# Optimization experiments

Measured on AMD Instinct MI355X. Metric: run time of the kernel, lower is better.

## Reference

```python
import jax, jax.numpy as jnp
import numpy as np

BLOCK = 64  # NF4 block size
SCALING = 32.0 / 16.0  # lora_alpha / r

# Standard NF4 (normal-float 4-bit) codebook, 16 levels
NF4_TABLE = jnp.asarray([
    -1.0, -0.6961928009986877, -0.5250730514526367, -0.39491748809814453,
    -0.28444138169288635, -0.18477343022823334, -0.09105003625154495, 0.0,
    0.07958029955625534, 0.16093020141124725, 0.24611230194568634,
    0.33791524171829224, 0.44070982933044434, 0.5626170039176941,
    0.7229568362236023, 1.0], dtype=jnp.float32)


def dequant_nf4(codes, scales):
    # codes: [out, in] int in [0,16); scales: [out, in//BLOCK] float
    out_f, in_f = codes.shape
    w = NF4_TABLE[codes].reshape(out_f, in_f // BLOCK, BLOCK)
    w = w * scales[:, :, None]
    return w.reshape(out_f, in_f)


def setup_inputs() -> dict:
    key = jax.random.key(0)
    k1, k2, k3, k4, k5 = jax.random.split(key, 5)
    B, S, D_in, D_out, R = 4, 2048, 4096, 4096, 16
    x = jax.random.normal(k1, (B, S, D_in), dtype=jnp.float32)
    codes = jax.random.randint(k2, (D_out, D_in), 0, 16, dtype=jnp.int32)
    scales = jax.random.uniform(k3, (D_out, D_in // BLOCK), dtype=jnp.float32)
    lora_A = jax.random.normal(k4, (R, D_in), dtype=jnp.float32) * (1.0 / np.sqrt(D_in))
    lora_B = jax.random.normal(k5, (D_out, R), dtype=jnp.float32) * 0.02
    return {"x": x, "codes": codes, "scales": scales,
            "lora_A": lora_A, "lora_B": lora_B}


def reference(x, codes, scales, lora_A, lora_B):
    # Base path: F.linear(x, dequant(W))  -> x @ W^T
    W = dequant_nf4(codes, scales)            # [out, in]
    base = jnp.einsum('bsd,od->bso', x, W)    # [B, S, out]
    # LoRA path (dropout p=0.0 -> identity): (x @ A^T) @ B^T * scaling
    lora = jnp.einsum('bsr,or->bso', jnp.einsum('bsd,rd->bsr', x, lora_A), lora_B)
    return base + lora * SCALING
```

## Files before the change

### kernel.cpp

```cpp
#include <hip/hip_runtime.h>
#include <hip/hip_bf16.h>

typedef __attribute__((ext_vector_type(8))) short short8;
typedef __attribute__((ext_vector_type(4))) short short4v;
typedef __attribute__((ext_vector_type(4))) float floatx4;

#define M_DIM 8192
#define N_DIM 4096
#define K_DIM 4096
#define BK 64

__device__ __constant__ float NF4_TAB[16] = {
    -1.0f, -0.6961928009986877f, -0.5250730514526367f, -0.39491748809814453f,
    -0.28444138169288635f, -0.18477343022823334f, -0.09105003625154495f, 0.0f,
    0.07958029955625534f, 0.16093020141124725f, 0.24611230194568634f,
    0.33791524171829224f, 0.44070982933044434f, 0.5626170039176941f,
    0.7229568362236023f, 1.0f};

__global__ __launch_bounds__(256)
void dequant_lora_kernel(const int* __restrict__ codes,
                         const float* __restrict__ scales,
                         const float* __restrict__ la,
                         const float* __restrict__ lb,
                         short4v* __restrict__ W) {
    __shared__ float tab[16];
    if (threadIdx.x < 16) tab[threadIdx.x] = NF4_TAB[threadIdx.x];
    __syncthreads();

    const int kb = blockIdx.x & 3;
    const int n0 = (blockIdx.x >> 2) << 4;
    const int k0 = kb * 1024 + threadIdx.x * 4;

    float4 a[16];
#pragma unroll
    for (int r = 0; r < 16; r++)
        a[r] = *(const float4*)(la + (size_t)r * K_DIM + k0);

#pragma unroll 4
    for (int i = 0; i < 16; i++) {
        const int n = n0 + i;
        int4 c = *(const int4*)(codes + (size_t)n * K_DIM + k0);
        float s = scales[(n << 6) + (k0 >> 6)];
        const float* bp = lb + (n << 4);
        float acc0 = 0.f, acc1 = 0.f, acc2 = 0.f, acc3 = 0.f;
#pragma unroll
        for (int r = 0; r < 16; r++) {
            float br = bp[r];
            acc0 += br * a[r].x;
            acc1 += br * a[r].y;
            acc2 += br * a[r].z;
            acc3 += br * a[r].w;
        }
        union { short4v v; __hip_bfloat16 h[4]; } u;
        u.h[0] = __float2bfloat16(tab[c.x] * s + 2.0f * acc0);
        u.h[1] = __float2bfloat16(tab[c.y] * s + 2.0f * acc1);
        u.h[2] = __float2bfloat16(tab[c.z] * s + 2.0f * acc2);
        u.h[3] = __float2bfloat16(tab[c.w] * s + 2.0f * acc3);
        W[((size_t)n * K_DIM + k0) >> 2] = u.v;
    }
}

__global__ void cast_x_kernel(const float* __restrict__ x,
                              short8* __restrict__ xb) {
    int g = blockIdx.x * blockDim.x + threadIdx.x;
    const float4* xp = (const float4*)(x + (size_t)g * 8);
    float4 v0 = xp[0], v1 = xp[1];
    union { short8 v; __hip_bfloat16 h[8]; } u;
    u.h[0] = __float2bfloat16(v0.x);
    u.h[1] = __float2bfloat16(v0.y);
    u.h[2] = __float2bfloat16(v0.z);
    u.h[3] = __float2bfloat16(v0.w);
    u.h[4] = __float2bfloat16(v1.x);
    u.h[5] = __float2bfloat16(v1.y);
    u.h[6] = __float2bfloat16(v1.z);
    u.h[7] = __float2bfloat16(v1.w);
    xb[g] = u.v;
}

#define GL2LDS(gsrc, ldst)                                                   \
    __builtin_amdgcn_global_load_lds(                                        \
        (const __attribute__((address_space(1))) void*)(gsrc),               \
        (__attribute__((address_space(3))) void*)(ldst), 16, 0, 0)


#define STAGE_A(D, H, T) do {                                                 \
    GL2LDS(gA0 + (size_t)((H) * 128) * K_DIM + (T) * BK,                      \
           ldsA + (D) * 32768 + (H) * 16384 + ldsw);                          \
    GL2LDS(gA0 + (size_t)((H) * 128 + 64) * K_DIM + (T) * BK,                 \
           ldsA + (D) * 32768 + (H) * 16384 + 8192 + ldsw);                   \
} while (0)

#define STAGE_B(D, H, T) do {                                                 \
    GL2LDS(gB0 + (size_t)((H) * 128) * K_DIM + (T) * BK,                      \
           ldsB + (D) * 32768 + (H) * 16384 + ldsw);                          \
    GL2LDS(gB0 + (size_t)((H) * 128 + 64) * K_DIM + (T) * BK,                 \
           ldsB + (D) * 32768 + (H) * 16384 + 8192 + ldsw);                   \
} while (0)

#define MFMA_Q(AF, BF, MB, NB) do {                                           \
    _Pragma("unroll") for (int mi_ = 0; mi_ < 4; mi_++)                       \
    _Pragma("unroll") for (int ni_ = 0; ni_ < 2; ni_++)                       \
    _Pragma("unroll") for (int ks_ = 0; ks_ < 2; ks_++)                       \
        acc[(MB) + mi_][(NB) + ni_] =                                         \
            __builtin_amdgcn_mfma_f32_16x16x32_bf16(                          \
                AF[mi_][ks_], BF[ni_][ks_], acc[(MB) + mi_][(NB) + ni_],      \
                0, 0, 0);                                                     \
} while (0)

#define LGKM0 asm volatile("s_waitcnt lgkmcnt(0)" ::: "memory")
#define VM4   asm volatile("s_waitcnt vmcnt(4)" ::: "memory")
#define VM0   asm volatile("s_waitcnt vmcnt(0)" ::: "memory")
#define VMNONE do {} while (0)

#define TILE(T, D, DOB, DOA, VM) do {                                         \
    short8 af0[4][2], af1[4][2], bf0[2][2], bf1[2][2];                        \
                                 \
    _Pragma("unroll") for (int mi_ = 0; mi_ < 4; mi_++) {                     \
        int o_ = (D) * 32768 + aoff + mi_ * 2048;                             \
        af0[mi_][0] = *(const short8*)(ldsA + o_);                            \
        af0[mi_][1] = *(const short8*)(ldsA + (o_ ^ 64));                     \
    }                                                                         \
    _Pragma("unroll") for (int ni_ = 0; ni_ < 2; ni_++) {                     \
        int o_ = (D) * 32768 + boff + ni_ * 2048;                             \
        bf0[ni_][0] = *(const short8*)(ldsB + o_);                            \
        bf0[ni_][1] = *(const short8*)(ldsB + (o_ ^ 64));                     \
    }                                                                         \
    if (DOB) STAGE_B((D) ^ 1, 0, (T) + 1);                                    \
    __builtin_amdgcn_s_barrier();                                             \
    LGKM0;                                                                    \
    __builtin_amdgcn_s_setprio(1);                                            \
    MFMA_Q(af0, bf0, 0, 0);                                                   \
    __builtin_amdgcn_s_setprio(0);                                            \
    __builtin_amdgcn_s_barrier();                                             \
                                          \
    _Pragma("unroll") for (int mi_ = 0; mi_ < 4; mi_++) {                     \
        int o_ = (D) * 32768 + aoff + 8192 + mi_ * 2048;                      \
        af1[mi_][0] = *(const short8*)(ldsA + o_);                            \
        af1[mi_][1] = *(const short8*)(ldsA + (o_ ^ 64));                     \
    }                                                                         \
    if (DOB) STAGE_B((D) ^ 1, 1, (T) + 1);                                    \
    __builtin_amdgcn_s_barrier();                                             \
    LGKM0;                                                                    \
    __builtin_amdgcn_s_setprio(1);                                            \
    MFMA_Q(af1, bf0, 4, 0);                                                   \
    __builtin_amdgcn_s_setprio(0);                                            \
    __builtin_amdgcn_s_barrier();                                             \
                                          \
    _Pragma("unroll") for (int ni_ = 0; ni_ < 2; ni_++) {                     \
        int o_ = (D) * 32768 + boff + 4096 + ni_ * 2048;                      \
        bf1[ni_][0] = *(const short8*)(ldsB + o_);                            \
        bf1[ni_][1] = *(const short8*)(ldsB + (o_ ^ 64));                     \
    }                                                                         \
    if (DOA) STAGE_A((D), 0, (T) + 2);                                        \
    __builtin_amdgcn_s_barrier();                                             \
    LGKM0;                                                                    \
    __builtin_amdgcn_s_setprio(1);                                            \
    MFMA_Q(af0, bf1, 0, 2);                                                   \
    __builtin_amdgcn_s_setprio(0);                                            \
    __builtin_amdgcn_s_barrier();                                             \
                       \
    if (DOA) STAGE_A((D), 1, (T) + 2);                                        \
    VM;                                                                       \
    __builtin_amdgcn_s_barrier();                                             \
    __builtin_amdgcn_s_setprio(1);                                            \
    MFMA_Q(af1, bf1, 4, 2);                                                   \
    __builtin_amdgcn_s_setprio(0);                                            \
    __builtin_amdgcn_s_barrier();                                             \
} while (0)

__global__ __launch_bounds__(512, 2)
void gemm_bt_kernel(const __hip_bfloat16* __restrict__ A,
                    const __hip_bfloat16* __restrict__ B,
                    float* __restrict__ C) {
    __shared__ __align__(16) char lds[131072];
    char* ldsA = (char*)lds;
    char* ldsB = (char*)lds + 65536;

    const int tid = threadIdx.x;
    const int wave = tid >> 6;
    const int lane = tid & 63;
    const int q = lane >> 4;
    const int t16 = lane & 15;
    const int wm = wave >> 2;
    const int wn = wave & 3;

    const int bid = blockIdx.x;
    const int swz = ((bid & 7) << 6) | (bid >> 3);
    const int bm0 = (swz >> 4) << 8;
    const int bn0 = (swz & 15) << 8;

    const int sw = (q ^ (t16 & 7)) << 4;
    const int aoff = (wm * 128 + t16) * 128 + sw;
    const int boff = (wn * 64 + t16) * 128 + sw;

    const int r0 = tid >> 3;
    const int c0 = ((tid & 7) ^ (r0 & 7)) << 3;
    const __hip_bfloat16* gA0 = A + (size_t)(bm0 + r0) * K_DIM + c0;
    const __hip_bfloat16* gB0 = B + (size_t)(bn0 + r0) * K_DIM + c0;
    const int ldsw = wave << 10;

    floatx4 acc[8][4] = {};

    STAGE_A(0, 0, 0); STAGE_A(0, 1, 0);
    STAGE_B(0, 0, 0); STAGE_B(0, 1, 0);
    STAGE_A(1, 0, 1); STAGE_A(1, 1, 1);
    VM4;
    __builtin_amdgcn_s_barrier();

#pragma unroll 1
    for (int tp = 0; tp < 31; ++tp) {
        const int t2 = tp << 1;
        TILE(t2, 0, 1, 1, VM4);
        TILE(t2 + 1, 1, 1, 1, VM4);
    }
    TILE(62, 0, 1, 0, VM0);
    TILE(63, 1, 0, 0, VMNONE);

#pragma unroll
    for (int mi = 0; mi < 8; mi++) {
        int row0 = bm0 + wm * 128 + mi * 16 + q * 4;
#pragma unroll
        for (int ni = 0; ni < 4; ni++) {
            int col = bn0 + wn * 64 + ni * 16 + t16;
            float* cp = C + (size_t)row0 * N_DIM + col;
#pragma unroll
            for (int r = 0; r < 4; r++) cp[(size_t)r * N_DIM] = acc[mi][ni][r];
        }
    }
}

extern "C" void kernel_launch(void* const* d_in, const int* in_sizes, int n_in,
                              void* d_out, int out_size, void* d_ws,
                              size_t ws_size, hipStream_t stream) {
    const float* x = (const float*)d_in[0];
    const int* codes = (const int*)d_in[1];
    const float* scales = (const float*)d_in[2];
    const float* loraA = (const float*)d_in[3];
    const float* loraB = (const float*)d_in[4];
    float* out = (float*)d_out;

    char* ws = (char*)d_ws;
    __hip_bfloat16* xb = (__hip_bfloat16*)ws;
    __hip_bfloat16* Wb = (__hip_bfloat16*)(ws + 67108864);

    dequant_lora_kernel<<<dim3(4 * (N_DIM / 16)), dim3(256), 0, stream>>>(
        codes, scales, loraA, loraB, (short4v*)Wb);
    cast_x_kernel<<<dim3((M_DIM * (K_DIM / 8)) / 256), dim3(256), 0, stream>>>(
        x, (short8*)xb);
    gemm_bt_kernel<<<dim3(512), dim3(512), 0, stream>>>(xb, Wb, out);
}
```

Before: 483.6 us.

## Prefetch next-tile LDS fragments in GEMM and merge prep kernels into one launch

The GEMM main loop now reads the next tile's first A and B fragments from LDS during the last MFMA quarter of the current tile. Each quarter's fragment read is moved one phase earlier, and the explicit lgkmcnt(0) waits are removed, so LDS latency can overlap MFMA work. The fragment registers are hoisted out of the tile macro so they persist across tiles, which raises register pressure. Separately, the dequant+LoRA kernel and the x-to-bf16 cast are merged into a single launch that branches on block index, saving one kernel launch and letting the two parts run concurrently.

After: 565.1 us. 16.9% more time.

```diff
diff --git a/kernel.cpp b/kernel.cpp
--- a/kernel.cpp
+++ b/kernel.cpp
@@ -18,63 +18,63 @@
     0.7229568362236023f, 1.0f};
 
 __global__ __launch_bounds__(256)
-void dequant_lora_kernel(const int* __restrict__ codes,
-                         const float* __restrict__ scales,
-                         const float* __restrict__ la,
-                         const float* __restrict__ lb,
-                         short4v* __restrict__ W) {
+void prep_kernel(const float* __restrict__ x, short8* __restrict__ xb,
+                 const int* __restrict__ codes,
+                 const float* __restrict__ scales,
+                 const float* __restrict__ la, const float* __restrict__ lb,
+                 short4v* __restrict__ W) {
     __shared__ float tab[16];
-    if (threadIdx.x < 16) tab[threadIdx.x] = NF4_TAB[threadIdx.x];
-    __syncthreads();
-
-    const int kb = blockIdx.x & 3;
-    const int n0 = (blockIdx.x >> 2) << 4;
-    const int k0 = kb * 1024 + threadIdx.x * 4;
-
-    float4 a[16];
-#pragma unroll
-    for (int r = 0; r < 16; r++)
-        a[r] = *(const float4*)(la + (size_t)r * K_DIM + k0);
+    const int bid = blockIdx.x;
+    if (bid < 1024) {
+        if (threadIdx.x < 16) tab[threadIdx.x] = NF4_TAB[threadIdx.x];
+        __syncthreads();
+
+        const int kb = bid & 3;
+        const int n0 = (bid >> 2) << 4;
+        const int k0 = kb * 1024 + threadIdx.x * 4;
+
+        float4 a[16];
+#pragma unroll
+        for (int r = 0; r < 16; r++)
+            a[r] = *(const float4*)(la + (size_t)r * K_DIM + k0);
 
 #pragma unroll 4
-    for (int i = 0; i < 16; i++) {
-        const int n = n0 + i;
-        int4 c = *(const int4*)(codes + (size_t)n * K_DIM + k0);
-        float s = scales[(n << 6) + (k0 >> 6)];
-        const float* bp = lb + (n << 4);
-        float acc0 = 0.f, acc1 = 0.f, acc2 = 0.f, acc3 = 0.f;
-#pragma unroll
-        for (int r = 0; r < 16; r++) {
-            float br = bp[r];
-            acc0 += br * a[r].x;
-            acc1 += br * a[r].y;
-            acc2 += br * a[r].z;
-            acc3 += br * a[r].w;
+        for (int i = 0; i < 16; i++) {
+            const int n = n0 + i;
+            int4 c = *(const int4*)(codes + (size_t)n * K_DIM + k0);
+            float s = scales[(n << 6) + (k0 >> 6)];
+            const float* bp = lb + (n << 4);
+            float acc0 = 0.f, acc1 = 0.f, acc2 = 0.f, acc3 = 0.f;
+#pragma unroll
+            for (int r = 0; r < 16; r++) {
+                float br = bp[r];
+                acc0 += br * a[r].x;
+                acc1 += br * a[r].y;
+                acc2 += br * a[r].z;
+                acc3 += br * a[r].w;
+            }
+            union { short4v v; __hip_bfloat16 h[4]; } u;
+            u.h[0] = __float2bfloat16(tab[c.x] * s + 2.0f * acc0);
+            u.h[1] = __float2bfloat16(tab[c.y] * s + 2.0f * acc1);
+            u.h[2] = __float2bfloat16(tab[c.z] * s + 2.0f * acc2);
+            u.h[3] = __float2bfloat16(tab[c.w] * s + 2.0f * acc3);
+            W[((size_t)n * K_DIM + k0) >> 2] = u.v;
         }
-        union { short4v v; __hip_bfloat16 h[4]; } u;
-        u.h[0] = __float2bfloat16(tab[c.x] * s + 2.0f * acc0);
-        u.h[1] = __float2bfloat16(tab[c.y] * s + 2.0f * acc1);
-        u.h[2] = __float2bfloat16(tab[c.z] * s + 2.0f * acc2);
-        u.h[3] = __float2bfloat16(tab[c.w] * s + 2.0f * acc3);
-        W[((size_t)n * K_DIM + k0) >> 2] = u.v;
+    } else {
+        const int g = (bid - 1024) * 256 + threadIdx.x;
+        const float4* xp = (const float4*)(x + (size_t)g * 8);
+        float4 v0 = xp[0], v1 = xp[1];
+        union { short8 v; __hip_bfloat16 h[8]; } u;
+        u.h[0] = __float2bfloat16(v0.x);
+        u.h[1] = __float2bfloat16(v0.y);
+        u.h[2] = __float2bfloat16(v0.z);
+        u.h[3] = __float2bfloat16(v0.w);
+        u.h[4] = __float2bfloat16(v1.x);
+        u.h[5] = __float2bfloat16(v1.y);
+        u.h[6] = __float2bfloat16(v1.z);
+        u.h[7] = __float2bfloat16(v1.w);
+        xb[g] = u.v;
     }
-}
-
-__global__ void cast_x_kernel(const float* __restrict__ x,
-                              short8* __restrict__ xb) {
-    int g = blockIdx.x * blockDim.x + threadIdx.x;
-    const float4* xp = (const float4*)(x + (size_t)g * 8);
-    float4 v0 = xp[0], v1 = xp[1];
-    union { short8 v; __hip_bfloat16 h[8]; } u;
-    u.h[0] = __float2bfloat16(v0.x);
-    u.h[1] = __float2bfloat16(v0.y);
-    u.h[2] = __float2bfloat16(v0.z);
-    u.h[3] = __float2bfloat16(v0.w);
-    u.h[4] = __float2bfloat16(v1.x);
-    u.h[5] = __float2bfloat16(v1.y);
-    u.h[6] = __float2bfloat16(v1.z);
-    u.h[7] = __float2bfloat16(v1.w);
-    xb[g] = u.v;
 }
 
 #define GL2LDS(gsrc, ldst)                                                   \
@@ -95,6 +95,38 @@
            ldsB + (D) * 32768 + (H) * 16384 + ldsw);                          \
     GL2LDS(gB0 + (size_t)((H) * 128 + 64) * K_DIM + (T) * BK,                 \
            ldsB + (D) * 32768 + (H) * 16384 + 8192 + ldsw);                   \
+} while (0)
+
+#define READ_AF0(D) do {                                                      \
+    _Pragma("unroll") for (int mi_ = 0; mi_ < 4; mi_++) {                     \
+        int o_ = (D) * 32768 + aoff + mi_ * 2048;                             \
+        af0[mi_][0] = *(const short8*)(ldsA + o_);                            \
+        af0[mi_][1] = *(const short8*)(ldsA + (o_ ^ 64));                     \
+    }                                                                         \
+} while (0)
+
+#define READ_AF1(D) do {                                                      \
+    _Pragma("unroll") for (int mi_ = 0; mi_ < 4; mi_++) {                     \
+        int o_ = (D) * 32768 + aoff + 8192 + mi_ * 2048;                      \
+        af1[mi_][0] = *(const short8*)(ldsA + o_);                            \
+        af1[mi_][1] = *(const short8*)(ldsA + (o_ ^ 64));                     \
+    }                                                                         \
+} while (0)
+
+#define READ_BF0(D) do {                                                      \
+    _Pragma("unroll") for (int ni_ = 0; ni_ < 2; ni_++) {                     \
+        int o_ = (D) * 32768 + boff + ni_ * 2048;                             \
+        bf0[ni_][0] = *(const short8*)(ldsB + o_);                            \
+        bf0[ni_][1] = *(const short8*)(ldsB + (o_ ^ 64));                     \
+    }                                                                         \
+} while (0)
+
+#define READ_BF1(D) do {                                                      \
+    _Pragma("unroll") for (int ni_ = 0; ni_ < 2; ni_++) {                     \
+        int o_ = (D) * 32768 + boff + 4096 + ni_ * 2048;                      \
+        bf1[ni_][0] = *(const short8*)(ldsB + o_);                            \
+        bf1[ni_][1] = *(const short8*)(ldsB + (o_ ^ 64));                     \
+    }                                                                         \
 } while (0)
 
 #define MFMA_Q(AF, BF, MB, NB) do {                                           \
@@ -107,61 +139,35 @@
                 0, 0, 0);                                                     \
 } while (0)
 
-#define LGKM0 asm volatile("s_waitcnt lgkmcnt(0)" ::: "memory")
 #define VM4   asm volatile("s_waitcnt vmcnt(4)" ::: "memory")
 #define VM0   asm volatile("s_waitcnt vmcnt(0)" ::: "memory")
 #define VMNONE do {} while (0)
 
-#define TILE(T, D, DOB, DOA, VM) do {                                         \
-    short8 af0[4][2], af1[4][2], bf0[2][2], bf1[2][2];                        \
-                                 \
-    _Pragma("unroll") for (int mi_ = 0; mi_ < 4; mi_++) {                     \
-        int o_ = (D) * 32768 + aoff + mi_ * 2048;                             \
-        af0[mi_][0] = *(const short8*)(ldsA + o_);                            \
-        af0[mi_][1] = *(const short8*)(ldsA + (o_ ^ 64));                     \
-    }                                                                         \
-    _Pragma("unroll") for (int ni_ = 0; ni_ < 2; ni_++) {                     \
-        int o_ = (D) * 32768 + boff + ni_ * 2048;                             \
-        bf0[ni_][0] = *(const short8*)(ldsB + o_);                            \
-        bf0[ni_][1] = *(const short8*)(ldsB + (o_ ^ 64));                     \
-    }                                                                         \
+#define TILE(T, D, DOB, DOA, VM, DOPF) do {                                   \
+    READ_AF1(D);                                                              \
     if (DOB) STAGE_B((D) ^ 1, 0, (T) + 1);                                    \
     __builtin_amdgcn_s_barrier();                                             \
-    LGKM0;                                                                    \
     __builtin_amdgcn_s_setprio(1);                                            \
     MFMA_Q(af0, bf0, 0, 0);                                                   \
     __builtin_amdgcn_s_setprio(0);                                            \
     __builtin_amdgcn_s_barrier();                                             \
-                                          \
-    _Pragma("unroll") for (int mi_ = 0; mi_ < 4; mi_++) {                     \
-        int o_ = (D) * 32768 + aoff + 8192 + mi_ * 2048;                      \
-        af1[mi_][0] = *(const short8*)(ldsA + o_);                            \
-        af1[mi_][1] = *(const short8*)(ldsA + (o_ ^ 64));                     \
-    }                                                                         \
+    READ_BF1(D);                                                              \
     if (DOB) STAGE_B((D) ^ 1, 1, (T) + 1);                                    \
     __builtin_amdgcn_s_barrier();                                             \
-    LGKM0;                                                                    \
     __builtin_amdgcn_s_setprio(1);                                            \
     MFMA_Q(af1, bf0, 4, 0);                                                   \
     __builtin_amdgcn_s_setprio(0);                                            \
     __builtin_amdgcn_s_barrier();                                             \
-                                          \
-    _Pragma("unroll") for (int ni_ = 0; ni_ < 2; ni_++) {                     \
-        int o_ = (D) * 32768 + boff + 4096 + ni_ * 2048;                      \
-        bf1[ni_][0] = *(const short8*)(ldsB + o_);                            \
-        bf1[ni_][1] = *(const short8*)(ldsB + (o_ ^ 64));                     \
-    }                                                                         \
     if (DOA) STAGE_A((D), 0, (T) + 2);                                        \
     __builtin_amdgcn_s_barrier();                                             \
-    LGKM0;                                                                    \
     __builtin_amdgcn_s_setprio(1);                                            \
     MFMA_Q(af0, bf1, 0, 2);                                                   \
     __builtin_amdgcn_s_setprio(0);                                            \
     __builtin_amdgcn_s_barrier();                                             \
-                       \
     if (DOA) STAGE_A((D), 1, (T) + 2);                                        \
     VM;                                                                       \
     __builtin_amdgcn_s_barrier();                                             \
+    if (DOPF) { READ_AF0((D) ^ 1); READ_BF0((D) ^ 1); }                       \
     __builtin_amdgcn_s_setprio(1);                                            \
     MFMA_Q(af1, bf1, 4, 2);                                                   \
     __builtin_amdgcn_s_setprio(0);                                            \
@@ -200,21 +206,24 @@
     const int ldsw = wave << 10;
 
     floatx4 acc[8][4] = {};
+    short8 af0[4][2], af1[4][2], bf0[2][2], bf1[2][2];
 
     STAGE_A(0, 0, 0); STAGE_A(0, 1, 0);
     STAGE_B(0, 0, 0); STAGE_B(0, 1, 0);
     STAGE_A(1, 0, 1); STAGE_A(1, 1, 1);
     VM4;
     __builtin_amdgcn_s_barrier();
+    READ_AF0(0);
+    READ_BF0(0);
 
 #pragma unroll 1
     for (int tp = 0; tp < 31; ++tp) {
         const int t2 = tp << 1;
-        TILE(t2, 0, 1, 1, VM4);
-        TILE(t2 + 1, 1, 1, 1, VM4);
+        TILE(t2, 0, 1, 1, VM4, 1);
+        TILE(t2 + 1, 1, 1, 1, VM4, 1);
     }
-    TILE(62, 0, 1, 0, VM0);
-    TILE(63, 1, 0, 0, VMNONE);
+    TILE(62, 0, 1, 0, VM0, 1);
+    TILE(63, 1, 0, 0, VMNONE, 0);
 
 #pragma unroll
     for (int mi = 0; mi < 8; mi++) {
@@ -243,9 +252,7 @@
     __hip_bfloat16* xb = (__hip_bfloat16*)ws;
     __hip_bfloat16* Wb = (__hip_bfloat16*)(ws + 67108864);
 
-    dequant_lora_kernel<<<dim3(4 * (N_DIM / 16)), dim3(256), 0, stream>>>(
-        codes, scales, loraA, loraB, (short4v*)Wb);
-    cast_x_kernel<<<dim3((M_DIM * (K_DIM / 8)) / 256), dim3(256), 0, stream>>>(
-        x, (short8*)xb);
+    prep_kernel<<<dim3(1024 + 16384), dim3(256), 0, stream>>>(
+        x, (short8*)xb, codes, scales, loraA, loraB, (short4v*)Wb);
     gemm_bt_kernel<<<dim3(512), dim3(512), 0, stream>>>(xb, Wb, out);
 }
```
